# Kernel optimization log

Measured on AMD Instinct MI355X. Metric: run time of the kernel, lower is better.

Reference implementation:

```python
import jax, jax.numpy as jnp
import numpy as np

B, S = 1, 2048
HIDDEN = 2560
NH, NKV, HD = 32, 8, 128
GS = 128  # awq group size
ROPE_THETA = 1000000.0


def dequant_q4(qweight, scales, qzeros):
    """Unpack int4 AWQ weights -> dense [K, N] float weight.
    qweight: [K//8, N] int32, 8 nibbles packed along the input (K) dim.
    scales/qzeros: [K//GS, N]. w = (nibble - zero) * scale.
    """
    K8, N = qweight.shape
    shifts = jnp.arange(8, dtype=jnp.int32) * 4
    nib = (qweight[:, None, :] >> shifts[None, :, None]) & 0xF  # [K//8, 8, N]
    w = nib.reshape(K8 * 8, N).astype(scales.dtype)             # [K, N]
    z = jnp.repeat(qzeros.astype(scales.dtype), GS, axis=0)     # [K, N]
    s = jnp.repeat(scales, GS, axis=0)                          # [K, N]
    return (w - z) * s


def linear_q4(x, qw, sc, qz, bias=None):
    w = dequant_q4(qw, sc, qz)                     # [K, N]
    y = jnp.einsum('bsk,kn->bsn', x, w)
    return y + bias if bias is not None else y


def rotate_half(x):
    x1, x2 = jnp.split(x, 2, axis=-1)
    return jnp.concatenate([-x2, x1], axis=-1)


def apply_rope(q, k, cos, sin):
    # cos/sin: [B, S, HD] -> broadcast over heads at dim 2
    c = cos[:, :, None, :]
    s = sin[:, :, None, :]
    return q * c + rotate_half(q) * s, k * c + rotate_half(k) * s


def setup_inputs() -> dict:
    key = jax.random.key(0)
    ks = jax.random.split(key, 12)

    x = jax.random.normal(ks[0], (B, S, HIDDEN), dtype=jnp.float32)

    # genuine rotary embedding tables
    inv_freq = 1.0 / (ROPE_THETA ** (np.arange(0, HD, 2, dtype=np.float32) / HD))
    t = np.arange(S, dtype=np.float32)
    freqs = np.outer(t, inv_freq)                      # [S, HD/2]
    emb = np.concatenate([freqs, freqs], axis=-1)      # [S, HD]
    cos = jnp.asarray(np.cos(emb)[None], dtype=jnp.float32)  # [1, S, HD]
    sin = jnp.asarray(np.sin(emb)[None], dtype=jnp.float32)

    def mk_proj(kq, ksc, kz, K, N, group=GS):
        qw = jax.random.randint(kq, (K // 8, N), 0, 2**31 - 1, dtype=jnp.int32)
        sc = jax.random.normal(ksc, (K // group, N), dtype=jnp.float32) * 0.01
        qz = jax.random.randint(kz, (K // group, N), 0, 16, dtype=jnp.int32)
        return qw, sc, qz

    q_qweight, q_scales, q_qzeros = mk_proj(ks[1], ks[2], ks[3], HIDDEN, NH * HD)
    k_qweight, k_scales, k_qzeros = mk_proj(ks[4], ks[5], ks[6], HIDDEN, NKV * HD)
    v_qweight, v_scales, v_qzeros = mk_proj(ks[7], ks[8], ks[9], HIDDEN, NKV * HD)
    o_qweight, o_scales, o_qzeros = mk_proj(ks[10], ks[11], jax.random.fold_in(key, 99), NH * HD, HIDDEN)

    kb = jax.random.split(jax.random.fold_in(key, 7), 3)
    q_bias = jax.random.normal(kb[0], (NH * HD,), dtype=jnp.float32) * 0.02
    k_bias = jax.random.normal(kb[1], (NKV * HD,), dtype=jnp.float32) * 0.02
    v_bias = jax.random.normal(kb[2], (NKV * HD,), dtype=jnp.float32) * 0.02

    return dict(x=x, cos=cos, sin=sin,
                q_scales=q_scales, q_bias=q_bias,
                k_scales=k_scales, k_bias=k_bias,
                v_scales=v_scales, v_bias=v_bias,
                o_scales=o_scales,
                q_qweight=q_qweight, q_qzeros=q_qzeros,
                k_qweight=k_qweight, k_qzeros=k_qzeros,
                v_qweight=v_qweight, v_qzeros=v_qzeros,
                o_qweight=o_qweight, o_qzeros=o_qzeros)


def reference(x, cos, sin,
              q_scales, q_bias, k_scales, k_bias, v_scales, v_bias, o_scales,
              q_qweight, q_qzeros, k_qweight, k_qzeros,
              v_qweight, v_qzeros, o_qweight, o_qzeros):
    b, s, _ = x.shape
    xq = linear_q4(x, q_qweight, q_scales, q_qzeros, q_bias).reshape(b, s, NH, HD)
    xk = linear_q4(x, k_qweight, k_scales, k_qzeros, k_bias).reshape(b, s, NKV, HD)
    xv = linear_q4(x, v_qweight, v_scales, v_qzeros, v_bias).reshape(b, s, NKV, HD)

    xq, xk = apply_rope(xq, xk, cos, sin)

    # GQA: repeat KV heads to match query heads (prefill, start_pos=0)
    rep = NH // NKV
    xk = jnp.repeat(xk, rep, axis=2)   # [b, s, NH, HD]
    xv = jnp.repeat(xv, rep, axis=2)

    scale = 1.0 / jnp.sqrt(jnp.asarray(HD, dtype=xq.dtype))
    scores = jnp.einsum('bqhd,bkhd->bhqk', xq, xk) * scale  # [b, NH, s, s]
    causal = jnp.tril(jnp.ones((s, s), dtype=bool))
    scores = jnp.where(causal[None, None], scores, jnp.finfo(scores.dtype).min)
    attn = jax.nn.softmax(scores, axis=-1)
    out = jnp.einsum('bhqk,bkhd->bqhd', attn, xv).reshape(b, s, NH * HD)

    return linear_q4(out, o_qweight, o_scales, o_qzeros)  # [b, s, HIDDEN]
```

## Files before the change

### kernel.cpp

```cpp
#include <hip/hip_runtime.h>
#include <hip/hip_bf16.h>
#include <cstdint>

#define S_LEN 2048
#define HIDDEN 2560
#define NH 32
#define NKV 8
#define HD 128
#define GS 128

typedef __attribute__((ext_vector_type(8))) _Float16 half8v;
typedef __attribute__((ext_vector_type(2))) _Float16 half2v;
typedef __attribute__((ext_vector_type(4))) float f32x4;
typedef unsigned int uint;
typedef unsigned short ushort;

__device__ inline ushort f2h(float f) {
    _Float16 h = (_Float16)f;
    return __builtin_bit_cast(ushort, h);
}
__device__ inline float h2f(ushort u) {
    return (float)__builtin_bit_cast(_Float16, u);
}
__device__ inline uint pk2(ushort a, ushort b) { return (uint)a | ((uint)b << 16); }

__device__ __attribute__((always_inline)) inline void gl_lds16(const void* g, void* l) {
    __builtin_amdgcn_global_load_lds(
        (const __attribute__((address_space(1))) unsigned int*)g,
        (__attribute__((address_space(3))) unsigned int*)l, 16, 0, 0);
}

__global__ __launch_bounds__(320) void xcvt_kernel(
    const float* __restrict__ X, ushort* __restrict__ Xf)
{
    const int row = blockIdx.x;
    const int t   = threadIdx.x;
    const size_t base = (size_t)row * HIDDEN + t * 8;
    float4 a = *(const float4*)&X[base];
    float4 b = *(const float4*)&X[base + 4];
    uint4 hw = {pk2(f2h(a.x), f2h(a.y)), pk2(f2h(a.z), f2h(a.w)),
                pk2(f2h(b.x), f2h(b.y)), pk2(f2h(b.z), f2h(b.w))};
    *(uint4*)&Xf[base] = hw;
}

__global__ __launch_bounds__(256) void qkv6_kernel(
    const ushort* __restrict__ Xf,
    const int* __restrict__ q_qw, const float* __restrict__ q_sc,
    const int* __restrict__ q_qz, const float* __restrict__ q_b,
    const int* __restrict__ k_qw, const float* __restrict__ k_sc,
    const int* __restrict__ k_qz, const float* __restrict__ k_b,
    const int* __restrict__ v_qw, const float* __restrict__ v_sc,
    const int* __restrict__ v_qz, const float* __restrict__ v_b,
    const float* __restrict__ cosb, const float* __restrict__ sinb,
    ushort* __restrict__ Qf, ushort* __restrict__ Kf,
    ushort* __restrict__ Vrm)
{
    __shared__ __align__(16) char LDSB[49152];
    ushort* A0 = (ushort*)(LDSB);
    ushort* A1 = (ushort*)(LDSB + 16384);
    ushort* Bt = (ushort*)(LDSB + 32768);

    const int t  = threadIdx.x;
    const int w  = t >> 6;
    const int l  = t & 63;
    const int lg = l >> 4;
    const int lr = l & 15;
    const int wr = w >> 1;
    const int wc = w & 1;
    const int K  = HIDDEN;

    const int bid = blockIdx.x;
    const int swz = (bid & 7) * 96 + (bid >> 3);
    const int nblk = swz % 48;
    const int m0   = (swz / 48) * 128;

    int region, nbase, Nw;
    const int* QW; const float* SC; const int* QZ; const float* BI;
    if (nblk < 32)      { region = 0; nbase = nblk * 128;        Nw = NH * HD;
                          QW = q_qw; SC = q_sc; QZ = q_qz; BI = q_b; }
    else if (nblk < 40) { region = 1; nbase = (nblk - 32) * 128; Nw = NKV * HD;
                          QW = k_qw; SC = k_sc; QZ = k_qz; BI = k_b; }
    else                { region = 2; nbase = (nblk - 40) * 128; Nw = NKV * HD;
                          QW = v_qw; SC = v_sc; QZ = v_qz; BI = v_b; }

    const int ldsAw = w * 1024;
    size_t aoff[4];
#pragma unroll
    for (int i = 0; i < 4; ++i) {
        int slot = i * 256 + t;
        int am = slot >> 3, ac = slot & 7;
        aoff[i] = (size_t)(m0 + am) * K + (size_t)((ac ^ (am & 7)) * 8);
    }
    const int bn  = t & 127;
    const int bk0 = (t >> 7) * 4;
    int bwoff[4];
#pragma unroll
    for (int j = 0; j < 4; ++j)
        bwoff[j] = (bn * 128 + (bk0 + j) * 16) ^ ((bn & 7) << 4);

    int ncm[4];
#pragma unroll
    for (int nf = 0; nf < 4; ++nf)
        ncm[nf] = wc * 32 + (nf & 1) * 16 + lr + ((nf & 2) ? 64 : 0);

    const int xorA = (lr & 7) << 4;
    int aroff[4][2], broff[4][2];
#pragma unroll
    for (int mf = 0; mf < 4; ++mf)
#pragma unroll
        for (int ks = 0; ks < 2; ++ks)
            aroff[mf][ks] = (((wr * 64 + mf * 16 + lr) * 128) + lg * 16 + ks * 64) ^ xorA;
#pragma unroll
    for (int nf = 0; nf < 4; ++nf)
#pragma unroll
        for (int ks = 0; ks < 2; ++ks)
            broff[nf][ks] = ((ncm[nf] * 128) + lg * 16 + ks * 64) ^ xorA;

    f32x4 macc[4][4];
#pragma unroll
    for (int mf = 0; mf < 4; ++mf)
#pragma unroll
        for (int nf = 0; nf < 4; ++nf) macc[mf][nf] = f32x4{0.f, 0.f, 0.f, 0.f};
    uint qr[4];
    float scf, zf;

#define QKV_QW(tile) { int g8 = (tile) * 8; int gg = (tile) >> 1; \
    _Pragma("unroll") \
    for (int j = 0; j < 4; ++j) \
        qr[j] = (uint)QW[(size_t)(g8 + bk0 + j) * Nw + nbase + bn]; \
    scf = SC[(size_t)gg * Nw + nbase + bn]; \
    zf  = (float)QZ[(size_t)gg * Nw + nbase + bn]; }

#define QKV_STAGE_A(AH, k0) { \
    gl_lds16(Xf + (k0) + aoff[0], (char*)(AH) + ldsAw); \
    gl_lds16(Xf + (k0) + aoff[1], (char*)(AH) + 4096 + ldsAw); \
    gl_lds16(Xf + (k0) + aoff[2], (char*)(AH) + 8192 + ldsAw); \
    gl_lds16(Xf + (k0) + aoff[3], (char*)(AH) + 12288 + ldsAw); }

#define QKV_BWRITE(BT) { \
    ushort sch = f2h(scf); \
    float schf = h2f(sch); \
    ushort msc = f2h(-128.0f * schf);    \
    ushort nzs = f2h(-(zf * schf)); \
    half2v S2 = {__builtin_bit_cast(_Float16, sch), __builtin_bit_cast(_Float16, sch)}; \
    half2v M2 = {__builtin_bit_cast(_Float16, msc), __builtin_bit_cast(_Float16, msc)}; \
    half2v Z2 = {__builtin_bit_cast(_Float16, nzs), __builtin_bit_cast(_Float16, nzs)}; \
    _Pragma("unroll") \
    for (int j = 0; j < 4; ++j) { \
        uint q = qr[j]; \
        uint b0 = q & 0xFFu, b1 = (q >> 8) & 0xFFu, b2 = (q >> 16) & 0xFFu, b3 = q >> 24; \
        uint e0 = 0x58005800u | ((b0 & 0xFu) << 3) | ((b0 & 0xF0u) << 15); \
        uint e1 = 0x58005800u | ((b1 & 0xFu) << 3) | ((b1 & 0xF0u) << 15); \
        uint e2 = 0x58005800u | ((b2 & 0xFu) << 3) | ((b2 & 0xF0u) << 15); \
        uint e3 = 0x58005800u | ((b3 & 0xFu) << 3) | ((b3 & 0xF0u) << 15); \
        half2v w0 = __builtin_bit_cast(half2v, e0) * S2 + M2; w0 = w0 + Z2; \
        half2v w1 = __builtin_bit_cast(half2v, e1) * S2 + M2; w1 = w1 + Z2; \
        half2v w2 = __builtin_bit_cast(half2v, e2) * S2 + M2; w2 = w2 + Z2; \
        half2v w3 = __builtin_bit_cast(half2v, e3) * S2 + M2; w3 = w3 + Z2; \
        uint4 dw = {__builtin_bit_cast(uint, w0), __builtin_bit_cast(uint, w1), \
                    __builtin_bit_cast(uint, w2), __builtin_bit_cast(uint, w3)}; \
        *(uint4*)((char*)(BT) + bwoff[j]) = dw; \
    } }

#define QKV_COMPUTE(AH, BT) { \
    _Pragma("unroll") \
    for (int ks = 0; ks < 2; ++ks) { \
        half8v av[4], bv[4]; \
        _Pragma("unroll") \
        for (int mf = 0; mf < 4; ++mf) \
            av[mf] = *(const half8v*)((const char*)(AH) + aroff[mf][ks]); \
        _Pragma("unroll") \
        for (int nf = 0; nf < 4; ++nf) \
            bv[nf] = *(const half8v*)((const char*)(BT) + broff[nf][ks]); \
        _Pragma("unroll") \
        for (int mf = 0; mf < 4; ++mf) \
            _Pragma("unroll") \
            for (int nf = 0; nf < 4; ++nf) \
                macc[mf][nf] = __builtin_amdgcn_mfma_f32_16x16x32_f16(av[mf], bv[nf], macc[mf][nf], 0, 0, 0); \
    } }

    QKV_QW(0);
    QKV_BWRITE(Bt);
    QKV_STAGE_A(A0, 0);
    QKV_QW(1);
    __syncthreads();

    for (int g = 0; g < 20; ++g) {
        QKV_COMPUTE(A0, Bt);
        __syncthreads();
        QKV_BWRITE(Bt);
        QKV_STAGE_A(A1, (2 * g + 1) * 64);
        if (g < 19) QKV_QW(2 * g + 2);
        __syncthreads();
        QKV_COMPUTE(A1, Bt);
        __syncthreads();
        if (g < 19) {
            QKV_BWRITE(Bt);
            QKV_STAGE_A(A0, (2 * g + 2) * 64);
            QKV_QW(2 * g + 3);
        }
        __syncthreads();
    }

#pragma unroll
    for (int nf = 0; nf < 4; ++nf) {
        float bv = BI[nbase + ncm[nf]];
#pragma unroll
        for (int mf = 0; mf < 4; ++mf)
#pragma unroll
            for (int r = 0; r < 4; ++r) macc[mf][nf][r] += bv;
    }

    if (region == 2) {
#pragma unroll
        for (int mf = 0; mf < 4; ++mf)
#pragma unroll
            for (int r = 0; r < 4; ++r) {
                int row = m0 + wr * 64 + mf * 16 + lg * 4 + r;
#pragma unroll
                for (int nf = 0; nf < 4; ++nf)
                    Vrm[(size_t)row * (NKV * HD) + nbase + ncm[nf]] = f2h(macc[mf][nf][r]);
            }
    } else {
        ushort* OF = (region == 0) ? Qf : Kf;
        const int No = (region == 0) ? NH * HD : NKV * HD;
        const float osc = (region == 0) ? 0.08838834764831845f : 1.0f;
#pragma unroll
        for (int mf = 0; mf < 4; ++mf)
#pragma unroll
            for (int r = 0; r < 4; ++r) {
                int row = m0 + wr * 64 + mf * 16 + lg * 4 + r;
                const float* cb = &cosb[(size_t)row * HD];
                const float* sb = &sinb[(size_t)row * HD];
#pragma unroll
                for (int nf = 0; nf < 2; ++nf) {
                    int d = wc * 32 + nf * 16 + lr;
                    float a = macc[mf][nf][r];
                    float b = macc[mf][nf + 2][r];
                    float o1 = (a * cb[d]      - b * sb[d])      * osc;
                    float o2 = (b * cb[d + 64] + a * sb[d + 64]) * osc;
                    OF[(size_t)row * No + nbase + d]      = f2h(o1);
                    OF[(size_t)row * No + nbase + d + 64] = f2h(o2);
                }
            }
    }
#undef QKV_QW
#undef QKV_STAGE_A
#undef QKV_BWRITE
#undef QKV_COMPUTE
}

__global__ __launch_bounds__(256) void vtrans_kernel(
    const ushort* __restrict__ Vrm, ushort* __restrict__ VfT)
{
    __shared__ ushort Ts[64][65];
    const int s0 = blockIdx.x * 64;
    const int n0 = blockIdx.y * 64;
    const int t  = threadIdx.x;
    {
        int r = t >> 2, c0 = (t & 3) * 16;
        uint4 v0 = *(const uint4*)&Vrm[(size_t)(s0 + r) * (NKV * HD) + n0 + c0];
        uint4 v1 = *(const uint4*)&Vrm[(size_t)(s0 + r) * (NKV * HD) + n0 + c0 + 8];
        const ushort* pv = (const ushort*)&v0;
#pragma unroll
        for (int j = 0; j < 8; ++j) Ts[r][c0 + j] = pv[j];
        pv = (const ushort*)&v1;
#pragma unroll
        for (int j = 0; j < 8; ++j) Ts[r][c0 + 8 + j] = pv[j];
    }
    __syncthreads();
    {
        int rn = t >> 2, cs0 = (t & 3) * 16;
        ushort ob[16];
#pragma unroll
        for (int j = 0; j < 16; ++j) ob[j] = Ts[cs0 + j][rn];
        ushort* dst = &VfT[(size_t)(n0 + rn) * S_LEN + s0 + cs0];
        *(uint4*)dst = ((uint4*)ob)[0];
        *(uint4*)(dst + 8) = ((uint4*)ob)[1];
    }
}

__global__ __launch_bounds__(256) void oproj5_kernel(
    const ushort* __restrict__ Xb, const int* __restrict__ QW,
    const float* __restrict__ SC, const int* __restrict__ QZ,
    float* __restrict__ Y)
{
    __shared__ __align__(16) char LDSB[49152];
    ushort* A0 = (ushort*)(LDSB);
    ushort* A1 = (ushort*)(LDSB + 16384);
    ushort* Bt = (ushort*)(LDSB + 32768);

    const int t  = threadIdx.x;
    const int w  = t >> 6;
    const int l  = t & 63;
    const int lg = l >> 4;
    const int lr = l & 15;
    const int wr = w >> 1;
    const int wc = w & 1;
    const int K  = NH * HD;
    const int N  = HIDDEN;

    const int bid = blockIdx.x;
    const int swz = (bid & 7) * 40 + (bid >> 3);
    const int n0  = (swz % 20) * 128;
    const int m0  = (swz / 20) * 128;

    const int ldsAw = w * 1024;
    size_t aoff[4];
#pragma unroll
    for (int i = 0; i < 4; ++i) {
        int slot = i * 256 + t;
        int am = slot >> 3, ac = slot & 7;
        aoff[i] = (size_t)(m0 + am) * K + (size_t)((ac ^ (am & 7)) * 8);
    }
    const int bn  = t & 127;
    const int bk0 = (t >> 7) * 4;
    int bwoff[4];
#pragma unroll
    for (int j = 0; j < 4; ++j)
        bwoff[j] = (bn * 128 + (bk0 + j) * 16) ^ ((bn & 7) << 4);

    const int xorA = (lr & 7) << 4;
    int aroff[4][2], broff[4][2];
#pragma unroll
    for (int mf = 0; mf < 4; ++mf)
#pragma unroll
        for (int ks = 0; ks < 2; ++ks)
            aroff[mf][ks] = (((wr * 64 + mf * 16 + lr) * 128) + lg * 16 + ks * 64) ^ xorA;
#pragma unroll
    for (int nf = 0; nf < 4; ++nf)
#pragma unroll
        for (int ks = 0; ks < 2; ++ks)
            broff[nf][ks] = (((wc * 64 + nf * 16 + lr) * 128) + lg * 16 + ks * 64) ^ xorA;

    f32x4 macc[4][4];
#pragma unroll
    for (int mf = 0; mf < 4; ++mf)
#pragma unroll
        for (int nf = 0; nf < 4; ++nf) macc[mf][nf] = f32x4{0.f, 0.f, 0.f, 0.f};
    uint qr[4];
    float scf, zf;

#define OP_QW(tile) { int g8 = (tile) * 8; int gg = (tile) >> 1; \
    _Pragma("unroll") \
    for (int j = 0; j < 4; ++j) \
        qr[j] = (uint)QW[(size_t)(g8 + bk0 + j) * N + n0 + bn]; \
    scf = SC[(size_t)gg * N + n0 + bn]; \
    zf  = (float)QZ[(size_t)gg * N + n0 + bn]; }

#define OP_STAGE_A(AH, k0) { \
    gl_lds16(Xb + (k0) + aoff[0], (char*)(AH) + ldsAw); \
    gl_lds16(Xb + (k0) + aoff[1], (char*)(AH) + 4096 + ldsAw); \
    gl_lds16(Xb + (k0) + aoff[2], (char*)(AH) + 8192 + ldsAw); \
    gl_lds16(Xb + (k0) + aoff[3], (char*)(AH) + 12288 + ldsAw); }

#define OP_BWRITE(BT) { \
    ushort sch = f2h(scf); \
    float schf = h2f(sch); \
    ushort msc = f2h(-128.0f * schf); \
    ushort nzs = f2h(-(zf * schf)); \
    half2v S2 = {__builtin_bit_cast(_Float16, sch), __builtin_bit_cast(_Float16, sch)}; \
    half2v M2 = {__builtin_bit_cast(_Float16, msc), __builtin_bit_cast(_Float16, msc)}; \
    half2v Z2 = {__builtin_bit_cast(_Float16, nzs), __builtin_bit_cast(_Float16, nzs)}; \
    _Pragma("unroll") \
    for (int j = 0; j < 4; ++j) { \
        uint q = qr[j]; \
        uint b0 = q & 0xFFu, b1 = (q >> 8) & 0xFFu, b2 = (q >> 16) & 0xFFu, b3 = q >> 24; \
        uint e0 = 0x58005800u | ((b0 & 0xFu) << 3) | ((b0 & 0xF0u) << 15); \
        uint e1 = 0x58005800u | ((b1 & 0xFu) << 3) | ((b1 & 0xF0u) << 15); \
        uint e2 = 0x58005800u | ((b2 & 0xFu) << 3) | ((b2 & 0xF0u) << 15); \
        uint e3 = 0x58005800u | ((b3 & 0xFu) << 3) | ((b3 & 0xF0u) << 15); \
        half2v w0 = __builtin_bit_cast(half2v, e0) * S2 + M2; w0 = w0 + Z2; \
        half2v w1 = __builtin_bit_cast(half2v, e1) * S2 + M2; w1 = w1 + Z2; \
        half2v w2 = __builtin_bit_cast(half2v, e2) * S2 + M2; w2 = w2 + Z2; \
        half2v w3 = __builtin_bit_cast(half2v, e3) * S2 + M2; w3 = w3 + Z2; \
        uint4 dw = {__builtin_bit_cast(uint, w0), __builtin_bit_cast(uint, w1), \
                    __builtin_bit_cast(uint, w2), __builtin_bit_cast(uint, w3)}; \
        *(uint4*)((char*)(BT) + bwoff[j]) = dw; \
    } }

#define OP_COMPUTE(AH, BT) { \
    _Pragma("unroll") \
    for (int ks = 0; ks < 2; ++ks) { \
        half8v av[4], bv[4]; \
        _Pragma("unroll") \
        for (int mf = 0; mf < 4; ++mf) \
            av[mf] = *(const half8v*)((const char*)(AH) + aroff[mf][ks]); \
        _Pragma("unroll") \
        for (int nf = 0; nf < 4; ++nf) \
            bv[nf] = *(const half8v*)((const char*)(BT) + broff[nf][ks]); \
        _Pragma("unroll") \
        for (int mf = 0; mf < 4; ++mf) \
            _Pragma("unroll") \
            for (int nf = 0; nf < 4; ++nf) \
                macc[mf][nf] = __builtin_amdgcn_mfma_f32_16x16x32_f16(av[mf], bv[nf], macc[mf][nf], 0, 0, 0); \
    } }

    OP_QW(0);
    OP_BWRITE(Bt);
    OP_STAGE_A(A0, 0);
    OP_QW(1);
    __syncthreads();

    for (int g = 0; g < 32; ++g) {
        OP_COMPUTE(A0, Bt);
        __syncthreads();
        OP_BWRITE(Bt);
        OP_STAGE_A(A1, (2 * g + 1) * 64);
        if (g < 31) OP_QW(2 * g + 2);
        __syncthreads();
        OP_COMPUTE(A1, Bt);
        __syncthreads();
        if (g < 31) {
            OP_BWRITE(Bt);
            OP_STAGE_A(A0, (2 * g + 2) * 64);
            OP_QW(2 * g + 3);
        }
        __syncthreads();
    }

#pragma unroll
    for (int mf = 0; mf < 4; ++mf)
#pragma unroll
        for (int r = 0; r < 4; ++r) {
            int row = m0 + wr * 64 + mf * 16 + lg * 4 + r;
#pragma unroll
            for (int nf = 0; nf < 4; ++nf)
                Y[(size_t)row * N + n0 + wc * 64 + nf * 16 + lr] = macc[mf][nf][r];
        }
#undef OP_QW
#undef OP_STAGE_A
#undef OP_BWRITE
#undef OP_COMPUTE
}

__global__ __launch_bounds__(256) void attn_mfma_kernel(
    const ushort* __restrict__ Qh,
    const ushort* __restrict__ Kh,
    const ushort* __restrict__ Vt,
    ushort* __restrict__ AO)
{
    __shared__ ushort KsF[32 * 128];
    __shared__ ushort Vs[128 * 32];
    __shared__ __align__(16) char PsB[4 * 1280];

    const int h  = blockIdx.x;
    const int qb = gridDim.y - 1 - blockIdx.y;
    const int s0 = qb * 64;
    const int t  = threadIdx.x;
    const int w  = t >> 6;
    const int l  = t & 63;
    const int lg = l >> 4;
    const int lr = l & 15;
    const int kvh = h >> 2;
    const int qw = s0 + w * 16;
    const int q  = qw + lr;

    half8v qf[4];
#pragma unroll
    for (int d = 0; d < 4; ++d) {
        size_t off = (size_t)q * (NH * HD) + h * HD + d * 32 + lg * 8;
        qf[d] = *(const half8v*)&Qh[off];
    }

    f32x4 o[8];
#pragma unroll
    for (int i = 0; i < 8; ++i) o[i] = f32x4{0.f, 0.f, 0.f, 0.f};
    float m = -1e30f, lsum = 0.f;
    char* pw = PsB + w * 1280;

    const int ntiles = qb * 2 + 2;
    for (int kt = 0; kt < ntiles; ++kt) {
        const int k0 = kt * 32;
#pragma unroll
        for (int i = 0; i < 2; ++i) {
            int slot = w * 128 + i * 64 + l;
            int mr = slot >> 4, c = slot & 15;
            size_t goff = (size_t)(k0 + mr) * (NKV * HD) + kvh * HD + ((c ^ (mr & 7)) * 8);
            gl_lds16(Kh + goff, (char*)KsF + (w * 128 + i * 64) * 16);
        }
#pragma unroll
        for (int i = 0; i < 2; ++i) {
            int slot = w * 128 + i * 64 + l;
            int dim = slot >> 2, c = slot & 3;
            size_t goff = (size_t)(kvh * HD + dim) * S_LEN + k0 + ((c ^ (dim & 3)) * 8);
            gl_lds16(Vt + goff, (char*)Vs + (w * 128 + i * 64) * 16);
        }
        __syncthreads();

        if (k0 <= qw + 15) {
            f32x4 s[2];
            s[0] = f32x4{0.f, 0.f, 0.f, 0.f};
            s[1] = f32x4{0.f, 0.f, 0.f, 0.f};
#pragma unroll
            for (int d = 0; d < 4; ++d) {
#pragma unroll
                for (int nt2 = 0; nt2 < 2; ++nt2) {
                    int row = nt2 * 16 + lr;
                    int off = row * 256 + ((d * 64 + lg * 16) ^ ((row & 7) << 4));
                    half8v kf = *(const half8v*)((char*)KsF + off);
                    s[nt2] = __builtin_amdgcn_mfma_f32_16x16x32_f16(kf, qf[d], s[nt2], 0, 0, 0);
                }
            }
            float sv[8];
#pragma unroll
            for (int nt2 = 0; nt2 < 2; ++nt2)
#pragma unroll
                for (int r = 0; r < 4; ++r) {
                    int kv = k0 + nt2 * 16 + lg * 4 + r;
                    sv[nt2 * 4 + r] = (kv <= q) ? s[nt2][r] : -1e30f;
                }
            float mx = sv[0];
#pragma unroll
            for (int j = 1; j < 8; ++j) mx = fmaxf(mx, sv[j]);
            mx = fmaxf(mx, __shfl_xor(mx, 16));
            mx = fmaxf(mx, __shfl_xor(mx, 32));
            float mnew = fmaxf(m, mx);
            float resc = __expf(m - mnew);
            m = mnew;
            float p[8], ps = 0.f;
#pragma unroll
            for (int j = 0; j < 8; ++j) { p[j] = __expf(sv[j] - mnew); ps += p[j]; }
            ps += __shfl_xor(ps, 16);
            ps += __shfl_xor(ps, 32);
            lsum = lsum * resc + ps;
#pragma unroll
            for (int dt = 0; dt < 8; ++dt)
#pragma unroll
                for (int r = 0; r < 4; ++r) o[dt][r] *= resc;
            uint2 w0 = {pk2(f2h(p[0]), f2h(p[1])), pk2(f2h(p[2]), f2h(p[3]))};
            uint2 w1 = {pk2(f2h(p[4]), f2h(p[5])), pk2(f2h(p[6]), f2h(p[7]))};
            *(uint2*)(pw + lr * 80 + lg * 8)      = w0;
            *(uint2*)(pw + lr * 80 + 32 + lg * 8) = w1;
            asm volatile("s_waitcnt lgkmcnt(0)" ::: "memory");
            half8v pf = *(const half8v*)(pw + lr * 80 + lg * 16);
#pragma unroll
            for (int dt = 0; dt < 8; ++dt) {
                int dim = dt * 16 + lr;
                half8v vf = *(const half8v*)((char*)Vs + dim * 64 + ((lg * 16) ^ ((dim & 3) << 4)));
                o[dt] = __builtin_amdgcn_mfma_f32_16x16x32_f16(vf, pf, o[dt], 0, 0, 0);
            }
        }
        __syncthreads();
    }

    float inv = 1.f / lsum;
    ushort* dst = &AO[(size_t)q * (NH * HD) + h * HD];
#pragma unroll
    for (int dt = 0; dt < 8; ++dt) {
        uint2 ov = {pk2(f2h(o[dt][0] * inv), f2h(o[dt][1] * inv)),
                    pk2(f2h(o[dt][2] * inv), f2h(o[dt][3] * inv))};
        *(uint2*)(dst + dt * 16 + lg * 4) = ov;
    }
}

extern "C" void kernel_launch(void* const* d_in, const int* in_sizes, int n_in,
                              void* d_out, int out_size, void* d_ws, size_t ws_size,
                              hipStream_t stream)
{
    const float* x    = (const float*)d_in[0];
    const float* cosb = (const float*)d_in[1];
    const float* sinb = (const float*)d_in[2];
    const float* q_sc = (const float*)d_in[3];
    const float* q_b  = (const float*)d_in[4];
    const float* k_sc = (const float*)d_in[5];
    const float* k_b  = (const float*)d_in[6];
    const float* v_sc = (const float*)d_in[7];
    const float* v_b  = (const float*)d_in[8];
    const float* o_sc = (const float*)d_in[9];
    const int* q_qw   = (const int*)d_in[10];
    const int* q_qz   = (const int*)d_in[11];
    const int* k_qw   = (const int*)d_in[12];
    const int* k_qz   = (const int*)d_in[13];
    const int* v_qw   = (const int*)d_in[14];
    const int* v_qz   = (const int*)d_in[15];
    const int* o_qw   = (const int*)d_in[16];
    const int* o_qz   = (const int*)d_in[17];
    float* out = (float*)d_out;

    char* ws = (char*)d_ws;
    ushort* Xf   = (ushort*)ws;
    ushort* AOf  = (ushort*)ws;
    ushort* Qf   = (ushort*)(ws + (size_t)16 * 1024 * 1024);
    ushort* Kf   = (ushort*)(ws + (size_t)32 * 1024 * 1024);
    ushort* Vrm  = (ushort*)(ws + (size_t)36 * 1024 * 1024);
    ushort* VfT  = (ushort*)(ws + (size_t)40 * 1024 * 1024);

    xcvt_kernel<<<S_LEN, 320, 0, stream>>>(x, Xf);

    qkv6_kernel<<<768, 256, 0, stream>>>(
        Xf,
        q_qw, q_sc, q_qz, q_b,
        k_qw, k_sc, k_qz, k_b,
        v_qw, v_sc, v_qz, v_b,
        cosb, sinb, Qf, Kf, Vrm);

    vtrans_kernel<<<dim3(S_LEN / 64, (NKV * HD) / 64), 256, 0, stream>>>(Vrm, VfT);

    attn_mfma_kernel<<<dim3(NH, S_LEN / 64), 256, 0, stream>>>(Qf, Kf, VfT, AOf);

    oproj5_kernel<<<320, 256, 0, stream>>>(
        AOf, o_qw, o_sc, o_qz, out);
}
```

Baseline: 287.2 us.

## Double-buffer dequantized B tiles and cut barriers in QKV and O-proj GEMMs

Both quantized GEMM kernels gain a second LDS buffer for the dequantized weight tile. The main loop now issues the next A-tile async load, computes, and writes the next B tile into the alternate buffer. Each half-iteration then ends with one raw barrier guarded by explicit lgkmcnt/vmcnt waits, replacing two __syncthreads. The aim is to halve barrier count and overlap staging with MFMA compute. In exchange LDS grows to 64KB per block, which may lower occupancy, and the hand-placed vmcnt counts risk races if they are miscounted.

```diff
diff --git a/kernel.cpp b/kernel.cpp
--- a/kernel.cpp
+++ b/kernel.cpp
@@ -29,6 +29,10 @@
         (const __attribute__((address_space(1))) unsigned int*)g,
         (__attribute__((address_space(3))) unsigned int*)l, 16, 0, 0);
 }
+
+#define WAIT_LGKM0  asm volatile("s_waitcnt lgkmcnt(0)" ::: "memory")
+#define WAIT_VM(N)  asm volatile("s_waitcnt vmcnt(" #N ")" ::: "memory")
+#define RAW_BARRIER { __builtin_amdgcn_s_barrier(); __builtin_amdgcn_sched_barrier(0); }
 
 __global__ __launch_bounds__(320) void xcvt_kernel(
     const float* __restrict__ X, ushort* __restrict__ Xf)
@@ -43,7 +47,7 @@
     *(uint4*)&Xf[base] = hw;
 }
 
-__global__ __launch_bounds__(256) void qkv6_kernel(
+__global__ __launch_bounds__(256) void qkv7_kernel(
     const ushort* __restrict__ Xf,
     const int* __restrict__ q_qw, const float* __restrict__ q_sc,
     const int* __restrict__ q_qz, const float* __restrict__ q_b,
@@ -55,10 +59,11 @@
     ushort* __restrict__ Qf, ushort* __restrict__ Kf,
     ushort* __restrict__ Vrm)
 {
-    __shared__ __align__(16) char LDSB[49152];
+    __shared__ __align__(16) char LDSB[65536];
     ushort* A0 = (ushort*)(LDSB);
     ushort* A1 = (ushort*)(LDSB + 16384);
-    ushort* Bt = (ushort*)(LDSB + 32768);
+    ushort* B0 = (ushort*)(LDSB + 32768);
+    ushort* B1 = (ushort*)(LDSB + 49152);
 
     const int t  = threadIdx.x;
     const int w  = t >> 6;
@@ -180,27 +185,36 @@
     } }
 
     QKV_QW(0);
-    QKV_BWRITE(Bt);
+    QKV_BWRITE(B0);
     QKV_STAGE_A(A0, 0);
     QKV_QW(1);
-    __syncthreads();
-
-    for (int g = 0; g < 20; ++g) {
-        QKV_COMPUTE(A0, Bt);
-        __syncthreads();
-        QKV_BWRITE(Bt);
+    WAIT_LGKM0;
+    WAIT_VM(6);
+    RAW_BARRIER;
+
+    for (int g = 0; g < 19; ++g) {
         QKV_STAGE_A(A1, (2 * g + 1) * 64);
-        if (g < 19) QKV_QW(2 * g + 2);
-        __syncthreads();
-        QKV_COMPUTE(A1, Bt);
-        __syncthreads();
-        if (g < 19) {
-            QKV_BWRITE(Bt);
-            QKV_STAGE_A(A0, (2 * g + 2) * 64);
-            QKV_QW(2 * g + 3);
-        }
-        __syncthreads();
-    }
+        QKV_COMPUTE(A0, B0);
+        QKV_BWRITE(B1);
+        QKV_QW(2 * g + 2);
+        WAIT_LGKM0;
+        WAIT_VM(6);
+        RAW_BARRIER;
+        QKV_STAGE_A(A0, (2 * g + 2) * 64);
+        QKV_COMPUTE(A1, B1);
+        QKV_BWRITE(B0);
+        QKV_QW(2 * g + 3);
+        WAIT_LGKM0;
+        WAIT_VM(6);
+        RAW_BARRIER;
+    }
+    QKV_STAGE_A(A1, 39 * 64);
+    QKV_COMPUTE(A0, B0);
+    QKV_BWRITE(B1);
+    WAIT_LGKM0;
+    WAIT_VM(0);
+    RAW_BARRIER;
+    QKV_COMPUTE(A1, B1);
 
 #pragma unroll
     for (int nf = 0; nf < 4; ++nf) {
@@ -280,15 +294,16 @@
     }
 }
 
-__global__ __launch_bounds__(256) void oproj5_kernel(
+__global__ __launch_bounds__(256) void oproj6_kernel(
     const ushort* __restrict__ Xb, const int* __restrict__ QW,
     const float* __restrict__ SC, const int* __restrict__ QZ,
     float* __restrict__ Y)
 {
-    __shared__ __align__(16) char LDSB[49152];
+    __shared__ __align__(16) char LDSB[65536];
     ushort* A0 = (ushort*)(LDSB);
     ushort* A1 = (ushort*)(LDSB + 16384);
-    ushort* Bt = (ushort*)(LDSB + 32768);
+    ushort* B0 = (ushort*)(LDSB + 32768);
+    ushort* B1 = (ushort*)(LDSB + 49152);
 
     const int t  = threadIdx.x;
     const int w  = t >> 6;
@@ -397,27 +412,36 @@
     } }
 
     OP_QW(0);
-    OP_BWRITE(Bt);
+    OP_BWRITE(B0);
     OP_STAGE_A(A0, 0);
     OP_QW(1);
-    __syncthreads();
-
-    for (int g = 0; g < 32; ++g) {
-        OP_COMPUTE(A0, Bt);
-        __syncthreads();
-        OP_BWRITE(Bt);
+    WAIT_LGKM0;
+    WAIT_VM(6);
+    RAW_BARRIER;
+
+    for (int g = 0; g < 31; ++g) {
         OP_STAGE_A(A1, (2 * g + 1) * 64);
-        if (g < 31) OP_QW(2 * g + 2);
-        __syncthreads();
-        OP_COMPUTE(A1, Bt);
-        __syncthreads();
-        if (g < 31) {
-            OP_BWRITE(Bt);
-            OP_STAGE_A(A0, (2 * g + 2) * 64);
-            OP_QW(2 * g + 3);
-        }
-        __syncthreads();
-    }
+        OP_COMPUTE(A0, B0);
+        OP_BWRITE(B1);
+        OP_QW(2 * g + 2);
+        WAIT_LGKM0;
+        WAIT_VM(6);
+        RAW_BARRIER;
+        OP_STAGE_A(A0, (2 * g + 2) * 64);
+        OP_COMPUTE(A1, B1);
+        OP_BWRITE(B0);
+        OP_QW(2 * g + 3);
+        WAIT_LGKM0;
+        WAIT_VM(6);
+        RAW_BARRIER;
+    }
+    OP_STAGE_A(A1, 63 * 64);
+    OP_COMPUTE(A0, B0);
+    OP_BWRITE(B1);
+    WAIT_LGKM0;
+    WAIT_VM(0);
+    RAW_BARRIER;
+    OP_COMPUTE(A1, B1);
 
 #pragma unroll
     for (int mf = 0; mf < 4; ++mf)
@@ -588,7 +612,7 @@
 
     xcvt_kernel<<<S_LEN, 320, 0, stream>>>(x, Xf);
 
-    qkv6_kernel<<<768, 256, 0, stream>>>(
+    qkv7_kernel<<<768, 256, 0, stream>>>(
         Xf,
         q_qw, q_sc, q_qz, q_b,
         k_qw, k_sc, k_qz, k_b,
@@ -599,6 +623,6 @@
 
     attn_mfma_kernel<<<dim3(NH, S_LEN / 64), 256, 0, stream>>>(Qf, Kf, VfT, AOf);
 
-    oproj5_kernel<<<320, 256, 0, stream>>>(
+    oproj6_kernel<<<320, 256, 0, stream>>>(
         AOf, o_qw, o_sc, o_qz, out);
 }
```

Result: faster. 265.6 us (-7.5%).
